# Performance work log

Measured on AMD Instinct MI355X. Metric: run time of the kernel, lower is better.

The kernel has to match this reference:

```python
import jax, jax.numpy as jnp
import numpy as np

BS, NQ, L = 64, 900, 1024
LANG_DIM, HID = 768, 256
N_EXP, TOP_K = 8, 2
MOE_W = 0.5
LOG_SCALE0 = 0.0
PRIOR_PROB = 0.01
BIAS0 = -np.log((1.0 - PRIOR_PROB) / PRIOR_PROB)  # -log((1-p)/p)


def setup_inputs() -> dict:
    key = jax.random.key(0)
    ks = jax.random.split(key, 8)
    s_in = 1.0 / np.sqrt(LANG_DIM)
    return {
        "x": jax.random.normal(ks[0], (BS, NQ, HID), jnp.float32),
        "embedding": jax.random.normal(ks[1], (BS, L, LANG_DIM), jnp.float32),
        "proj_w": jax.random.uniform(ks[2], (LANG_DIM, HID), jnp.float32, -s_in, s_in),
        "proj_b": jnp.zeros((HID,), jnp.float32),
        "gate_w": jax.random.uniform(ks[3], (LANG_DIM, N_EXP), jnp.float32, -s_in, s_in),
        "gate_b": jnp.zeros((N_EXP,), jnp.float32),
        "expert_w": jax.random.uniform(ks[4], (N_EXP, LANG_DIM, HID), jnp.float32, -s_in, s_in),
        "expert_b": jnp.zeros((N_EXP, HID), jnp.float32),
        "bias_lang": jnp.zeros((LANG_DIM,), jnp.float32),
        "bias0": jnp.array([BIAS0], jnp.float32),
        "log_scale": jnp.array([LOG_SCALE0], jnp.float32),
    }


def _moe(emb, gate_w, gate_b, expert_w, expert_b):
    # emb: (bs, L, lang_dim)
    gate_logits = emb @ gate_w + gate_b              # (bs, L, E)
    gate_weights = jax.nn.softmax(gate_logits, axis=-1)
    topv, topi = jax.lax.top_k(gate_weights, TOP_K)  # (bs, L, k)
    # dense combine weights: scatter top-k probs back to (bs, L, E)
    combine = jnp.sum(jax.nn.one_hot(topi, N_EXP, dtype=emb.dtype) * topv[..., None], axis=-2)
    out = jnp.zeros(emb.shape[:-1] + (HID,), emb.dtype)
    for e in range(N_EXP):  # small fixed expert count; dense per-expert GEMM
        out = out + combine[..., e:e + 1] * (emb @ expert_w[e] + expert_b[e])
    return out


def reference(x, embedding, proj_w, proj_b, gate_w, gate_b,
              expert_w, expert_b, bias_lang, bias0, log_scale):
    emb = embedding / jnp.linalg.norm(embedding, axis=-1, keepdims=True)
    tokens = emb @ proj_w + proj_b                        # (bs, L, HID)
    moe_out = _moe(emb, gate_w, gate_b, expert_w, expert_b)
    tokens = (1.0 - MOE_W) * tokens + MOE_W * moe_out
    token_bias = emb @ bias_lang + bias0[0]               # (bs, L)
    logit = jnp.einsum('bqh,blh->bql', x, tokens) / jnp.exp(log_scale[0])
    logit = logit + token_bias[:, None, :]
    logit = jnp.clip(logit, -50000.0, 50000.0)
    return logit
```

## Files before the change

### kernel.cpp

```cpp
#include <hip/hip_runtime.h>
#include <hip/hip_bf16.h>


typedef __attribute__((ext_vector_type(8))) short bf16x8;
typedef __attribute__((ext_vector_type(4))) float f32x4;

#define NROW 65536
#define CAP  65536
#define CSTRIDE 16

__device__ __forceinline__ unsigned short f2bf(float f) {
    unsigned u = __builtin_bit_cast(unsigned, f);
    u += 0x7fffu + ((u >> 16) & 1u);
    return (unsigned short)(u >> 16);
}
__device__ __forceinline__ float bf2f(unsigned short h) {
    unsigned u = ((unsigned)h) << 16;
    return __builtin_bit_cast(float, u);
}
__device__ __forceinline__ void gload16(const void* g, void* l) {
    __builtin_amdgcn_global_load_lds(
        (const __attribute__((address_space(1))) void*)g,
        (__attribute__((address_space(3))) void*)l, 16, 0, 0);
}
__device__ __forceinline__ unsigned cvt_pk_bf16(float a, float b) {
    unsigned r;
    asm("v_cvt_pk_bf16_f32 %0, %1, %2" : "=v"(r) : "v"(a), "v"(b));
    return r;
}

__global__ __launch_bounds__(256) void kx_cast(
    const float* __restrict__ x, unsigned short* __restrict__ x_bf)
{
    int i = blockIdx.x * 256 + threadIdx.x;
    float4 v = ((const float4*)x)[i];
    uint2 o = { cvt_pk_bf16(v.x, v.y), cvt_pk_bf16(v.z, v.w) };
    ((uint2*)x_bf)[i] = o;
}

__global__ __launch_bounds__(256) void k0_wT(
    const float* __restrict__ proj_w, const float* __restrict__ expert_w,
    unsigned short* __restrict__ wcatT)
{
    int j = blockIdx.z;
    int d0 = blockIdx.x * 64, h0 = blockIdx.y * 64;
    const float* W = (j < 8) ? expert_w + (size_t)j * 768 * 256 : proj_w;
    __shared__ unsigned short s[64][65];
    int t = threadIdx.x;
    #pragma unroll
    for (int i = 0; i < 16; i++) {
        int d = i * 4 + (t >> 6), h = t & 63;
        s[d][h] = f2bf(W[(size_t)(d0 + d) * 256 + h0 + h]);
    }
    __syncthreads();
    #pragma unroll
    for (int i = 0; i < 16; i++) {
        int h = i * 4 + (t >> 6), d = t & 63;
        wcatT[(size_t)(j * 256 + h0 + h) * 768 + d0 + d] = s[d][h];
    }
}

__global__ __launch_bounds__(256) void kz_misc(
    const float* __restrict__ proj_b, const float* __restrict__ expert_b,
    float* __restrict__ bcat, unsigned* __restrict__ cnt)
{
    int i = blockIdx.x * 256 + threadIdx.x;
    if (i < 2304) {
        int jj = i >> 8, h = i & 255;
        bcat[i] = (jj < 8) ? expert_b[jj * 256 + h] : proj_b[h];
    }
    if (i < 8 * CSTRIDE) cnt[i] = 0;
}

__global__ __launch_bounds__(256, 4) void k1_fused(
    const float* __restrict__ emb_in, const float* __restrict__ gate_w,
    const float* __restrict__ gate_b, const float* __restrict__ bias_lang,
    const float* __restrict__ bias0, unsigned short* __restrict__ emb_bf,
    unsigned* __restrict__ top2, float2* __restrict__ c2,
    float* __restrict__ tbias)
{
    __shared__ float gwT[9 * 768];
    for (int i = threadIdx.x; i < 768 * 8; i += 256) {
        int d = i >> 3, e = i & 7;
        gwT[e * 768 + d] = gate_w[i];
    }
    for (int i = threadIdx.x; i < 768; i += 256)
        gwT[8 * 768 + i] = bias_lang[i];
    __syncthreads();

    int w = threadIdx.x >> 6, lane = threadIdx.x & 63;
    #pragma unroll 1
    for (int it = 0; it < 8; ++it) {
        int r = blockIdx.x * 32 + w * 8 + it;
        const float4* rv = (const float4*)(emb_in + (size_t)r * 768);
        float4 v0 = rv[lane], v1 = rv[lane + 64], v2 = rv[lane + 128];
        float ss = v0.x*v0.x + v0.y*v0.y + v0.z*v0.z + v0.w*v0.w
                 + v1.x*v1.x + v1.y*v1.y + v1.z*v1.z + v1.w*v1.w
                 + v2.x*v2.x + v2.y*v2.y + v2.z*v2.z + v2.w*v2.w;
        #pragma unroll
        for (int m = 1; m < 64; m <<= 1) ss += __shfl_xor(ss, m, 64);
        float rn = rsqrtf(ss);

        uint2 o0 = { cvt_pk_bf16(v0.x*rn, v0.y*rn), cvt_pk_bf16(v0.z*rn, v0.w*rn) };
        uint2 o1 = { cvt_pk_bf16(v1.x*rn, v1.y*rn), cvt_pk_bf16(v1.z*rn, v1.w*rn) };
        uint2 o2 = { cvt_pk_bf16(v2.x*rn, v2.y*rn), cvt_pk_bf16(v2.z*rn, v2.w*rn) };
        uint2* ob = (uint2*)(emb_bf + (size_t)r * 768);
        ob[lane] = o0; ob[lane + 64] = o1; ob[lane + 128] = o2;

        float acc[9];
        #pragma unroll
        for (int i = 0; i < 9; i++) acc[i] = 0.f;
        const float4 vv[3] = { v0, v1, v2 };
        #pragma unroll
        for (int k = 0; k < 3; k++) {
            float4 v = vv[k];
            #pragma unroll
            for (int e = 0; e < 9; e++) {
                float4 g = *(const float4*)&gwT[e * 768 + k * 256 + lane * 4];
                acc[e] += v.x*g.x + v.y*g.y + v.z*g.z + v.w*g.w;
            }
        }
        #pragma unroll
        for (int m = 1; m < 64; m <<= 1) {
            #pragma unroll
            for (int i = 0; i < 9; i++) acc[i] += __shfl_xor(acc[i], m, 64);
        }
        if (lane == 0) {
            float g[8];
            #pragma unroll
            for (int e = 0; e < 8; e++) g[e] = acc[e] * rn + gate_b[e];
            float mx = g[0];
            #pragma unroll
            for (int e = 1; e < 8; e++) mx = fmaxf(mx, g[e]);
            float p[8], s = 0.f;
            #pragma unroll
            for (int e = 0; e < 8; e++) { p[e] = __expf(g[e] - mx); s += p[e]; }
            float inv = 0.5f / s;
            int i1 = 0;
            #pragma unroll
            for (int e = 1; e < 8; e++) if (g[e] > g[i1]) i1 = e;
            int i2 = (i1 == 0) ? 1 : 0;
            #pragma unroll
            for (int e = 0; e < 8; e++) if (e != i1 && g[e] > g[i2]) i2 = e;
            top2[r] = (unsigned)i1 | ((unsigned)i2 << 8);
            c2[r]   = make_float2(p[i1] * inv, p[i2] * inv);
            tbias[r] = acc[8] * rn + bias0[0];
        }
    }
}

__global__ __launch_bounds__(256) void kb_bucket(
    const unsigned* __restrict__ top2, const float2* __restrict__ c2,
    unsigned* __restrict__ cnt, unsigned* __restrict__ bidx,
    float* __restrict__ bscale)
{
    __shared__ unsigned lcnt[8];
    __shared__ unsigned gbase[8];
    int tid = threadIdx.x, lane = tid & 63;
    if (tid < 8) lcnt[tid] = 0;
    __syncthreads();
    int r = blockIdx.x * 256 + tid;
    unsigned t = top2[r];
    float2 c = c2[r];
    int ii[2] = { (int)(t & 255), (int)((t >> 8) & 255) };
    float cc[2] = { c.x, c.y };
    unsigned lpos[2];
    #pragma unroll
    for (int slot = 0; slot < 2; slot++) {
        int myE = ii[slot];
        #pragma unroll 1
        for (int e = 0; e < 8; e++) {
            unsigned long long mask = __ballot(myE == e);
            if (myE == e) {
                int leader = __ffsll((unsigned long long)mask) - 1;
                unsigned base = 0;
                if (lane == leader)
                    base = atomicAdd(&lcnt[e], (unsigned)__popcll(mask));
                base = __shfl(base, leader, 64);
                lpos[slot] = base + (unsigned)__popcll(mask & ((1ull << lane) - 1ull));
            }
        }
    }
    __syncthreads();
    if (tid < 8) gbase[tid] = atomicAdd(&cnt[tid * CSTRIDE], lcnt[tid]);
    __syncthreads();
    #pragma unroll
    for (int slot = 0; slot < 2; slot++) {
        int e = ii[slot];
        unsigned p = gbase[e] + lpos[slot];
        bidx[(size_t)e * CAP + p]   = (unsigned)r | ((unsigned)slot << 16);
        bscale[(size_t)e * CAP + p] = cc[slot];
    }
}

__global__ __launch_bounds__(512, 2) void k2_expert(
    const unsigned short* __restrict__ emb_bf, const unsigned short* __restrict__ wcatT,
    const float* __restrict__ bcat, const unsigned* __restrict__ cnt,
    const unsigned* __restrict__ bidx, const float* __restrict__ bscale,
    unsigned short* __restrict__ partial)
{
    int e = blockIdx.y;
    int tile = blockIdx.x;
    int cnt_e = (e < 8) ? (int)cnt[e * CSTRIDE] : NROW;
    if (tile * 128 >= cnt_e) return;
    int tid = threadIdx.x, lane = tid & 63, w = tid >> 6;
    int wm = w >> 2, wn = w & 3;
    __shared__ __align__(16) unsigned short As[2][128 * 32];
    __shared__ __align__(16) unsigned short Bs[2][256 * 32];
    __shared__ unsigned sRow[128];
    __shared__ float sScale[128];
    if (tid < 128) {
        int gi = tile * 128 + tid;
        unsigned rs; float sc;
        if (e == 8)           { rs = (unsigned)gi | (2u << 16); sc = 0.5f; }
        else if (gi < cnt_e)  { rs = bidx[(size_t)e * CAP + gi];
                                sc = bscale[(size_t)e * CAP + gi]; }
        else                  { rs = 0; sc = 0.f; }
        sRow[tid] = rs; sScale[tid] = sc;
    }
    __syncthreads();
    int r16 = lane & 15, r4 = lane >> 4;
    int srowA = tid >> 2, ssegA = (tid & 3) ^ (srowA & 3);
    const unsigned short* aSrc =
        emb_bf + (size_t)(sRow[srowA] & 0xFFFFu) * 768 + ssegA * 8;
    const unsigned short* bBase = wcatT + (size_t)e * 256 * 768;

    auto stageA = [&](int kt, int buf) {
        gload16(aSrc + kt * 32, &As[buf][w * 512]);
    };
    auto stageB = [&](int kt, int buf) {
        #pragma unroll
        for (int i = 0; i < 2; i++) {
            int u = i * 512 + tid;
            int brow = u >> 2, seg = (u & 3) ^ (brow & 3);
            gload16(&bBase[(size_t)brow * 768 + kt * 32 + seg * 8],
                    &Bs[buf][i * 4096 + w * 512]);
        }
    };

    f32x4 acc[4][4];
    #pragma unroll
    for (int mi = 0; mi < 4; mi++)
        #pragma unroll
        for (int ni = 0; ni < 4; ni++) acc[mi][ni] = f32x4{0.f, 0.f, 0.f, 0.f};

    stageA(0, 0); stageB(0, 0);
    __syncthreads();
    int buf = 0;
    #pragma unroll 1
    for (int kt = 0; kt < 24; ++kt) {
        if (kt < 23) { stageA(kt + 1, buf ^ 1); stageB(kt + 1, buf ^ 1); }
        bf16x8 a[4], b[4];
        #pragma unroll
        for (int mi = 0; mi < 4; mi++) {
            int arow = wm * 64 + mi * 16 + r16;
            a[mi] = *(const bf16x8*)&As[buf][arow * 32 + (r4 ^ (arow & 3)) * 8];
        }
        #pragma unroll
        for (int ni = 0; ni < 4; ni++) {
            int brow = wn * 64 + ni * 16 + r16;
            b[ni] = *(const bf16x8*)&Bs[buf][brow * 32 + (r4 ^ (brow & 3)) * 8];
        }
        #pragma unroll
        for (int mi = 0; mi < 4; mi++)
            #pragma unroll
            for (int ni = 0; ni < 4; ni++)
                acc[mi][ni] = __builtin_amdgcn_mfma_f32_16x16x32_bf16(
                    a[mi], b[ni], acc[mi][ni], 0, 0, 0);
        __syncthreads();
        buf ^= 1;
    }

    float bj[4];
    #pragma unroll
    for (int ni = 0; ni < 4; ni++) bj[ni] = bcat[e * 256 + wn * 64 + ni * 16 + r16];
    #pragma unroll
    for (int mi = 0; mi < 4; mi++) {
        #pragma unroll
        for (int e4 = 0; e4 < 4; e4++) {
            int rl = wm * 64 + mi * 16 + r4 * 4 + e4;
            if (tile * 128 + rl < cnt_e) {
                unsigned rs = sRow[rl];
                float sc = sScale[rl];
                unsigned rowg = rs & 0xFFFFu, slot = rs >> 16;
                #pragma unroll
                for (int ni = 0; ni < 4; ni++) {
                    int col = wn * 64 + ni * 16 + r16;
                    partial[((size_t)slot * NROW + rowg) * 256 + col] =
                        f2bf(sc * (acc[mi][ni][e4] + bj[ni]));
                }
            }
        }
    }
}

__global__ __launch_bounds__(256) void k2_combine(
    const unsigned short* __restrict__ partial, unsigned short* __restrict__ tokens)
{
    size_t i = ((size_t)blockIdx.x * 256 + threadIdx.x) * 8;
    const size_t S = (size_t)NROW * 256;
    bf16x8 p0 = *(const bf16x8*)&partial[i];
    bf16x8 p1 = *(const bf16x8*)&partial[S + i];
    bf16x8 p2 = *(const bf16x8*)&partial[2 * S + i];
    union { bf16x8 v; unsigned short s[8]; } o;
    #pragma unroll
    for (int e = 0; e < 8; e++)
        o.s[e] = f2bf(bf2f((unsigned short)p0[e]) + bf2f((unsigned short)p1[e]) +
                      bf2f((unsigned short)p2[e]));
    *(bf16x8*)&tokens[i] = o.v;
}

__global__ __launch_bounds__(256, 3) void k3_logit(
    const unsigned short* __restrict__ x_bf, const unsigned short* __restrict__ tokens,
    const float* __restrict__ tbias, const float* __restrict__ log_scale,
    float* __restrict__ out)
{
    int tid = threadIdx.x, lane = tid & 63, w = tid >> 6;
    int wm = w >> 1, wn = w & 1;
    int tn = blockIdx.x, tm = blockIdx.y, b = blockIdx.z;
    __shared__ __align__(16) unsigned short As[2][128 * 32];
    __shared__ __align__(16) unsigned short Bs[2][128 * 32];
    const unsigned short* A = x_bf + (size_t)b * 900 * 256;
    const unsigned short* B = tokens + (size_t)b * 1024 * 256;
    f32x4 acc[4][4];
    #pragma unroll
    for (int mi = 0; mi < 4; mi++)
        #pragma unroll
        for (int ni = 0; ni < 4; ni++) acc[mi][ni] = f32x4{0.f, 0.f, 0.f, 0.f};
    int r16 = lane & 15, r4 = lane >> 4;

    auto stage = [&](int kt, int buf) {
        #pragma unroll
        for (int i = 0; i < 2; i++) {
            int u = i * 256 + tid;
            int row = u >> 2, seg = (u & 3) ^ (row & 3);
            int ar = tm * 128 + row;
            if (ar > 899) ar = 899;
            gload16(&A[(size_t)ar * 256 + kt * 32 + seg * 8],
                    &As[buf][i * 2048 + w * 512]);
            int nr = tn * 128 + row;
            gload16(&B[(size_t)nr * 256 + kt * 32 + seg * 8],
                    &Bs[buf][i * 2048 + w * 512]);
        }
    };

    stage(0, 0);
    __syncthreads();
    int buf = 0;
    #pragma unroll 1
    for (int kt = 0; kt < 8; ++kt) {
        if (kt < 7) stage(kt + 1, buf ^ 1);
        bf16x8 a[4], bb[4];
        #pragma unroll
        for (int mi = 0; mi < 4; mi++) {
            int row = wm * 64 + mi * 16 + r16;
            a[mi] = *(const bf16x8*)&As[buf][row * 32 + (r4 ^ (row & 3)) * 8];
        }
        #pragma unroll
        for (int ni = 0; ni < 4; ni++) {
            int row = wn * 64 + ni * 16 + r16;
            bb[ni] = *(const bf16x8*)&Bs[buf][row * 32 + (r4 ^ (row & 3)) * 8];
        }
        #pragma unroll
        for (int mi = 0; mi < 4; mi++)
            #pragma unroll
            for (int ni = 0; ni < 4; ni++)
                acc[mi][ni] = __builtin_amdgcn_mfma_f32_16x16x32_bf16(
                    a[mi], bb[ni], acc[mi][ni], 0, 0, 0);
        __syncthreads();
        buf ^= 1;
    }
    float inv = __expf(-log_scale[0]);
    #pragma unroll
    for (int ni = 0; ni < 4; ni++) {
        int l = tn * 128 + wn * 64 + ni * 16 + r16;
        float tbv = tbias[b * 1024 + l];
        #pragma unroll
        for (int mi = 0; mi < 4; mi++) {
            #pragma unroll
            for (int e = 0; e < 4; e++) {
                int q = tm * 128 + wm * 64 + mi * 16 + r4 * 4 + e;
                if (q < 900) {
                    float vv = acc[mi][ni][e] * inv + tbv;
                    vv = fminf(fmaxf(vv, -50000.f), 50000.f);
                    out[((size_t)b * 900 + q) * 1024 + l] = vv;
                }
            }
        }
    }
}

extern "C" void kernel_launch(void* const* d_in, const int* in_sizes, int n_in,
                              void* d_out, int out_size, void* d_ws, size_t ws_size,
                              hipStream_t stream)
{
    const float* x         = (const float*)d_in[0];
    const float* embedding = (const float*)d_in[1];
    const float* proj_w    = (const float*)d_in[2];
    const float* proj_b    = (const float*)d_in[3];
    const float* gate_w    = (const float*)d_in[4];
    const float* gate_b    = (const float*)d_in[5];
    const float* expert_w  = (const float*)d_in[6];
    const float* expert_b  = (const float*)d_in[7];
    const float* bias_lang = (const float*)d_in[8];
    const float* bias0     = (const float*)d_in[9];
    const float* log_scale = (const float*)d_in[10];
    float* out = (float*)d_out;

    size_t off = 0;
    char* base = (char*)d_ws;
    auto alloc = [&](size_t bytes) -> void* {
        void* p = base + off;
        off += (bytes + 255) & ~(size_t)255;
        return p;
    };
    unsigned short* emb_bf  = (unsigned short*)alloc((size_t)NROW * 768 * 2);
    unsigned short* x_bf    = (unsigned short*)alloc((size_t)14745600 * 2);
    unsigned short* wcatT   = (unsigned short*)alloc((size_t)2304 * 768 * 2);
    float* bcat             = (float*)alloc(2304 * 4);
    float* tbias            = (float*)alloc((size_t)NROW * 4);
    unsigned short* tokens  = (unsigned short*)alloc((size_t)NROW * 256 * 2);
    unsigned* cnt           = (unsigned*)alloc(8 * CSTRIDE * 4);
    unsigned* top2          = (unsigned*)alloc((size_t)NROW * 4);
    float2* c2              = (float2*)alloc((size_t)NROW * 8);
    unsigned* bidx          = (unsigned*)alloc((size_t)8 * CAP * 4);
    float* bscale           = (float*)alloc((size_t)8 * CAP * 4);
    unsigned short* partial = (unsigned short*)alloc((size_t)3 * NROW * 256 * 2);

    kx_cast<<<14400, 256, 0, stream>>>(x, x_bf);
    dim3 gt(12, 4, 9);
    k0_wT<<<gt, 256, 0, stream>>>(proj_w, expert_w, wcatT);
    kz_misc<<<9, 256, 0, stream>>>(proj_b, expert_b, bcat, cnt);
    k1_fused<<<2048, 256, 0, stream>>>(embedding, gate_w, gate_b, bias_lang, bias0,
                                       emb_bf, top2, c2, tbias);
    kb_bucket<<<NROW / 256, 256, 0, stream>>>(top2, c2, cnt, bidx, bscale);
    dim3 g2(512, 9);
    k2_expert<<<g2, 512, 0, stream>>>(emb_bf, wcatT, bcat, cnt, bidx, bscale, partial);
    k2_combine<<<8192, 256, 0, stream>>>(partial, tokens);
    dim3 g3(8, 8, 64);
    k3_logit<<<g3, 256, 0, stream>>>(x_bf, tokens, tbias, log_scale, out);
}
```

Measured before the change: 395.9 us.

## Triple-buffer LDS staging with partial vmcnt waits in expert and logit GEMMs

Both GEMM kernels move from double- to triple-buffered LDS tiles, prefetching two K-steps ahead. The full __syncthreads is replaced by a partial s_waitcnt vmcnt plus s_barrier, so the next tile's global-to-LDS loads can stay in flight across the barrier. This is meant to hide global load latency behind MFMA work. In exchange, LDS use per block grows by half, which may reduce occupancy (k2 goes to about 72KB per block), and the hand-coded vmcnt counts must match the number of issued loads exactly.

Result: slower. 415.3 us (+4.9%).

```diff
diff --git a/kernel.cpp b/kernel.cpp
--- a/kernel.cpp
+++ b/kernel.cpp
@@ -205,8 +205,8 @@
     if (tile * 128 >= cnt_e) return;
     int tid = threadIdx.x, lane = tid & 63, w = tid >> 6;
     int wm = w >> 2, wn = w & 3;
-    __shared__ __align__(16) unsigned short As[2][128 * 32];
-    __shared__ __align__(16) unsigned short Bs[2][256 * 32];
+    __shared__ __align__(16) unsigned short As[3][128 * 32];
+    __shared__ __align__(16) unsigned short Bs[3][256 * 32];
     __shared__ unsigned sRow[128];
     __shared__ float sScale[128];
     if (tid < 128) {
@@ -245,21 +245,25 @@
         for (int ni = 0; ni < 4; ni++) acc[mi][ni] = f32x4{0.f, 0.f, 0.f, 0.f};
 
     stageA(0, 0); stageB(0, 0);
-    __syncthreads();
-    int buf = 0;
+    stageA(1, 1); stageB(1, 1);
+    asm volatile("s_waitcnt vmcnt(3)" ::: "memory");
+    __builtin_amdgcn_s_barrier();
+
+    int rb = 0;
     #pragma unroll 1
     for (int kt = 0; kt < 24; ++kt) {
-        if (kt < 23) { stageA(kt + 1, buf ^ 1); stageB(kt + 1, buf ^ 1); }
+        int sb = rb + 2; if (sb >= 3) sb -= 3;
+        if (kt < 22) { stageA(kt + 2, sb); stageB(kt + 2, sb); }
         bf16x8 a[4], b[4];
         #pragma unroll
         for (int mi = 0; mi < 4; mi++) {
             int arow = wm * 64 + mi * 16 + r16;
-            a[mi] = *(const bf16x8*)&As[buf][arow * 32 + (r4 ^ (arow & 3)) * 8];
+            a[mi] = *(const bf16x8*)&As[rb][arow * 32 + (r4 ^ (arow & 3)) * 8];
         }
         #pragma unroll
         for (int ni = 0; ni < 4; ni++) {
             int brow = wn * 64 + ni * 16 + r16;
-            b[ni] = *(const bf16x8*)&Bs[buf][brow * 32 + (r4 ^ (brow & 3)) * 8];
+            b[ni] = *(const bf16x8*)&Bs[rb][brow * 32 + (r4 ^ (brow & 3)) * 8];
         }
         #pragma unroll
         for (int mi = 0; mi < 4; mi++)
@@ -267,8 +271,12 @@
             for (int ni = 0; ni < 4; ni++)
                 acc[mi][ni] = __builtin_amdgcn_mfma_f32_16x16x32_bf16(
                     a[mi], b[ni], acc[mi][ni], 0, 0, 0);
-        __syncthreads();
-        buf ^= 1;
+        if (kt < 23) {
+            if (kt == 22) asm volatile("s_waitcnt vmcnt(0)" ::: "memory");
+            else          asm volatile("s_waitcnt vmcnt(3)" ::: "memory");
+            __builtin_amdgcn_s_barrier();
+        }
+        rb = rb + 1; if (rb >= 3) rb = 0;
     }
 
     float bj[4];
@@ -318,8 +326,8 @@
     int tid = threadIdx.x, lane = tid & 63, w = tid >> 6;
     int wm = w >> 1, wn = w & 1;
     int tn = blockIdx.x, tm = blockIdx.y, b = blockIdx.z;
-    __shared__ __align__(16) unsigned short As[2][128 * 32];
-    __shared__ __align__(16) unsigned short Bs[2][128 * 32];
+    __shared__ __align__(16) unsigned short As[3][128 * 32];
+    __shared__ __align__(16) unsigned short Bs[3][128 * 32];
     const unsigned short* A = x_bf + (size_t)b * 900 * 256;
     const unsigned short* B = tokens + (size_t)b * 1024 * 256;
     f32x4 acc[4][4];
@@ -345,21 +353,25 @@
     };
 
     stage(0, 0);
-    __syncthreads();
-    int buf = 0;
+    stage(1, 1);
+    asm volatile("s_waitcnt vmcnt(4)" ::: "memory");
+    __builtin_amdgcn_s_barrier();
+
+    int rb = 0;
     #pragma unroll 1
     for (int kt = 0; kt < 8; ++kt) {
-        if (kt < 7) stage(kt + 1, buf ^ 1);
+        int sb = rb + 2; if (sb >= 3) sb -= 3;
+        if (kt < 6) stage(kt + 2, sb);
         bf16x8 a[4], bb[4];
         #pragma unroll
         for (int mi = 0; mi < 4; mi++) {
             int row = wm * 64 + mi * 16 + r16;
-            a[mi] = *(const bf16x8*)&As[buf][row * 32 + (r4 ^ (row & 3)) * 8];
+            a[mi] = *(const bf16x8*)&As[rb][row * 32 + (r4 ^ (row & 3)) * 8];
         }
         #pragma unroll
         for (int ni = 0; ni < 4; ni++) {
             int row = wn * 64 + ni * 16 + r16;
-            bb[ni] = *(const bf16x8*)&Bs[buf][row * 32 + (r4 ^ (row & 3)) * 8];
+            bb[ni] = *(const bf16x8*)&Bs[rb][row * 32 + (r4 ^ (row & 3)) * 8];
         }
         #pragma unroll
         for (int mi = 0; mi < 4; mi++)
@@ -367,8 +379,12 @@
             for (int ni = 0; ni < 4; ni++)
                 acc[mi][ni] = __builtin_amdgcn_mfma_f32_16x16x32_bf16(
                     a[mi], bb[ni], acc[mi][ni], 0, 0, 0);
-        __syncthreads();
-        buf ^= 1;
+        if (kt < 7) {
+            if (kt == 6) asm volatile("s_waitcnt vmcnt(0)" ::: "memory");
+            else         asm volatile("s_waitcnt vmcnt(4)" ::: "memory");
+            __builtin_amdgcn_s_barrier();
+        }
+        rb = rb + 1; if (rb >= 3) rb = 0;
     }
     float inv = __expf(-log_scale[0]);
     #pragma unroll
```

## Fuse projection GEMM with partial combine, add nontemporal stores and stronger LDS swizzle

Applied to the files above, without the earlier changes.

Removes the separate combine kernel by moving the projection GEMM (former expert slot 8) into a dedicated kernel that adds the two expert partials in its epilogue. This drops one partial buffer and a full read/write pass over the tokens. The change also widens the LDS XOR swizzle to mix in more row bits, makes the large output and intermediate writes nontemporal, and raises k3_logit occupancy to 4 blocks. The risks are a serialized projection kernel in place of one overlapped inside the expert grid, plus possible register pressure at the higher occupancy.

Result: no change. 393.8 us (-0.5%).

```diff
diff --git a/kernel.cpp b/kernel.cpp
--- a/kernel.cpp
+++ b/kernel.cpp
@@ -8,6 +8,7 @@
 #define NROW 65536
 #define CAP  65536
 #define CSTRIDE 16
+#define SWZ(r) ((((r) & 3) ^ (((r) >> 2) & 3)))
 
 __device__ __forceinline__ unsigned short f2bf(float f) {
     unsigned u = __builtin_bit_cast(unsigned, f);
@@ -34,8 +35,9 @@
 {
     int i = blockIdx.x * 256 + threadIdx.x;
     float4 v = ((const float4*)x)[i];
-    uint2 o = { cvt_pk_bf16(v.x, v.y), cvt_pk_bf16(v.z, v.w) };
-    ((uint2*)x_bf)[i] = o;
+    unsigned long long o = (unsigned long long)cvt_pk_bf16(v.x, v.y) |
+                           ((unsigned long long)cvt_pk_bf16(v.z, v.w) << 32);
+    __builtin_nontemporal_store(o, (unsigned long long*)x_bf + i);
 }
 
 __global__ __launch_bounds__(256) void k0_wT(
@@ -101,11 +103,16 @@
         for (int m = 1; m < 64; m <<= 1) ss += __shfl_xor(ss, m, 64);
         float rn = rsqrtf(ss);
 
-        uint2 o0 = { cvt_pk_bf16(v0.x*rn, v0.y*rn), cvt_pk_bf16(v0.z*rn, v0.w*rn) };
-        uint2 o1 = { cvt_pk_bf16(v1.x*rn, v1.y*rn), cvt_pk_bf16(v1.z*rn, v1.w*rn) };
-        uint2 o2 = { cvt_pk_bf16(v2.x*rn, v2.y*rn), cvt_pk_bf16(v2.z*rn, v2.w*rn) };
-        uint2* ob = (uint2*)(emb_bf + (size_t)r * 768);
-        ob[lane] = o0; ob[lane + 64] = o1; ob[lane + 128] = o2;
+        unsigned long long q0 = (unsigned long long)cvt_pk_bf16(v0.x*rn, v0.y*rn) |
+                                ((unsigned long long)cvt_pk_bf16(v0.z*rn, v0.w*rn) << 32);
+        unsigned long long q1 = (unsigned long long)cvt_pk_bf16(v1.x*rn, v1.y*rn) |
+                                ((unsigned long long)cvt_pk_bf16(v1.z*rn, v1.w*rn) << 32);
+        unsigned long long q2 = (unsigned long long)cvt_pk_bf16(v2.x*rn, v2.y*rn) |
+                                ((unsigned long long)cvt_pk_bf16(v2.z*rn, v2.w*rn) << 32);
+        unsigned long long* ob = (unsigned long long*)(emb_bf + (size_t)r * 768);
+        __builtin_nontemporal_store(q0, ob + lane);
+        __builtin_nontemporal_store(q1, ob + lane + 64);
+        __builtin_nontemporal_store(q2, ob + lane + 128);
 
         float acc[9];
         #pragma unroll
@@ -201,7 +208,7 @@
 {
     int e = blockIdx.y;
     int tile = blockIdx.x;
-    int cnt_e = (e < 8) ? (int)cnt[e * CSTRIDE] : NROW;
+    int cnt_e = (int)cnt[e * CSTRIDE];
     if (tile * 128 >= cnt_e) return;
     int tid = threadIdx.x, lane = tid & 63, w = tid >> 6;
     int wm = w >> 2, wn = w & 3;
@@ -212,15 +219,14 @@
     if (tid < 128) {
         int gi = tile * 128 + tid;
         unsigned rs; float sc;
-        if (e == 8)           { rs = (unsigned)gi | (2u << 16); sc = 0.5f; }
-        else if (gi < cnt_e)  { rs = bidx[(size_t)e * CAP + gi];
-                                sc = bscale[(size_t)e * CAP + gi]; }
-        else                  { rs = 0; sc = 0.f; }
+        if (gi < cnt_e) { rs = bidx[(size_t)e * CAP + gi];
+                          sc = bscale[(size_t)e * CAP + gi]; }
+        else            { rs = 0; sc = 0.f; }
         sRow[tid] = rs; sScale[tid] = sc;
     }
     __syncthreads();
     int r16 = lane & 15, r4 = lane >> 4;
-    int srowA = tid >> 2, ssegA = (tid & 3) ^ (srowA & 3);
+    int srowA = tid >> 2, ssegA = (tid & 3) ^ SWZ(srowA);
     const unsigned short* aSrc =
         emb_bf + (size_t)(sRow[srowA] & 0xFFFFu) * 768 + ssegA * 8;
     const unsigned short* bBase = wcatT + (size_t)e * 256 * 768;
@@ -232,7 +238,7 @@
         #pragma unroll
         for (int i = 0; i < 2; i++) {
             int u = i * 512 + tid;
-            int brow = u >> 2, seg = (u & 3) ^ (brow & 3);
+            int brow = u >> 2, seg = (u & 3) ^ SWZ(brow);
             gload16(&bBase[(size_t)brow * 768 + kt * 32 + seg * 8],
                     &Bs[buf][i * 4096 + w * 512]);
         }
@@ -254,12 +260,12 @@
         #pragma unroll
         for (int mi = 0; mi < 4; mi++) {
             int arow = wm * 64 + mi * 16 + r16;
-            a[mi] = *(const bf16x8*)&As[buf][arow * 32 + (r4 ^ (arow & 3)) * 8];
+            a[mi] = *(const bf16x8*)&As[buf][arow * 32 + (r4 ^ SWZ(arow)) * 8];
         }
         #pragma unroll
         for (int ni = 0; ni < 4; ni++) {
             int brow = wn * 64 + ni * 16 + r16;
-            b[ni] = *(const bf16x8*)&Bs[buf][brow * 32 + (r4 ^ (brow & 3)) * 8];
+            b[ni] = *(const bf16x8*)&Bs[buf][brow * 32 + (r4 ^ SWZ(brow)) * 8];
         }
         #pragma unroll
         for (int mi = 0; mi < 4; mi++)
@@ -286,31 +292,101 @@
                 #pragma unroll
                 for (int ni = 0; ni < 4; ni++) {
                     int col = wn * 64 + ni * 16 + r16;
-                    partial[((size_t)slot * NROW + rowg) * 256 + col] =
-                        f2bf(sc * (acc[mi][ni][e4] + bj[ni]));
+                    __builtin_nontemporal_store(
+                        f2bf(sc * (acc[mi][ni][e4] + bj[ni])),
+                        &partial[((size_t)slot * NROW + rowg) * 256 + col]);
                 }
             }
         }
     }
 }
 
-__global__ __launch_bounds__(256) void k2_combine(
-    const unsigned short* __restrict__ partial, unsigned short* __restrict__ tokens)
-{
-    size_t i = ((size_t)blockIdx.x * 256 + threadIdx.x) * 8;
+__global__ __launch_bounds__(512, 2) void k2_proj(
+    const unsigned short* __restrict__ emb_bf, const unsigned short* __restrict__ wcatT,
+    const float* __restrict__ bcat, const unsigned short* __restrict__ partial,
+    unsigned short* __restrict__ tokens)
+{
+    int tile = blockIdx.x;
+    int tid = threadIdx.x, lane = tid & 63, w = tid >> 6;
+    int wm = w >> 2, wn = w & 3;
+    int rowBase = tile * 128;
+    __shared__ __align__(16) unsigned short As[2][128 * 32];
+    __shared__ __align__(16) unsigned short Bs[2][256 * 32];
+    int r16 = lane & 15, r4 = lane >> 4;
+    int srowA = tid >> 2, ssegA = (tid & 3) ^ SWZ(srowA);
+    const unsigned short* aSrc =
+        emb_bf + (size_t)(rowBase + srowA) * 768 + ssegA * 8;
+    const unsigned short* bBase = wcatT + (size_t)8 * 256 * 768;
+
+    auto stageA = [&](int kt, int buf) {
+        gload16(aSrc + kt * 32, &As[buf][w * 512]);
+    };
+    auto stageB = [&](int kt, int buf) {
+        #pragma unroll
+        for (int i = 0; i < 2; i++) {
+            int u = i * 512 + tid;
+            int brow = u >> 2, seg = (u & 3) ^ SWZ(brow);
+            gload16(&bBase[(size_t)brow * 768 + kt * 32 + seg * 8],
+                    &Bs[buf][i * 4096 + w * 512]);
+        }
+    };
+
+    f32x4 acc[4][4];
+    #pragma unroll
+    for (int mi = 0; mi < 4; mi++)
+        #pragma unroll
+        for (int ni = 0; ni < 4; ni++) acc[mi][ni] = f32x4{0.f, 0.f, 0.f, 0.f};
+
+    stageA(0, 0); stageB(0, 0);
+    __syncthreads();
+    int buf = 0;
+    #pragma unroll 1
+    for (int kt = 0; kt < 24; ++kt) {
+        if (kt < 23) { stageA(kt + 1, buf ^ 1); stageB(kt + 1, buf ^ 1); }
+        bf16x8 a[4], b[4];
+        #pragma unroll
+        for (int mi = 0; mi < 4; mi++) {
+            int arow = wm * 64 + mi * 16 + r16;
+            a[mi] = *(const bf16x8*)&As[buf][arow * 32 + (r4 ^ SWZ(arow)) * 8];
+        }
+        #pragma unroll
+        for (int ni = 0; ni < 4; ni++) {
+            int brow = wn * 64 + ni * 16 + r16;
+            b[ni] = *(const bf16x8*)&Bs[buf][brow * 32 + (r4 ^ SWZ(brow)) * 8];
+        }
+        #pragma unroll
+        for (int mi = 0; mi < 4; mi++)
+            #pragma unroll
+            for (int ni = 0; ni < 4; ni++)
+                acc[mi][ni] = __builtin_amdgcn_mfma_f32_16x16x32_bf16(
+                    a[mi], b[ni], acc[mi][ni], 0, 0, 0);
+        __syncthreads();
+        buf ^= 1;
+    }
+
     const size_t S = (size_t)NROW * 256;
-    bf16x8 p0 = *(const bf16x8*)&partial[i];
-    bf16x8 p1 = *(const bf16x8*)&partial[S + i];
-    bf16x8 p2 = *(const bf16x8*)&partial[2 * S + i];
-    union { bf16x8 v; unsigned short s[8]; } o;
-    #pragma unroll
-    for (int e = 0; e < 8; e++)
-        o.s[e] = f2bf(bf2f((unsigned short)p0[e]) + bf2f((unsigned short)p1[e]) +
-                      bf2f((unsigned short)p2[e]));
-    *(bf16x8*)&tokens[i] = o.v;
-}
-
-__global__ __launch_bounds__(256, 3) void k3_logit(
+    float bj[4];
+    #pragma unroll
+    for (int ni = 0; ni < 4; ni++) bj[ni] = bcat[8 * 256 + wn * 64 + ni * 16 + r16];
+    #pragma unroll
+    for (int mi = 0; mi < 4; mi++) {
+        #pragma unroll
+        for (int e4 = 0; e4 < 4; e4++) {
+            int rl = wm * 64 + mi * 16 + r4 * 4 + e4;
+            size_t rowg = rowBase + rl;
+            #pragma unroll
+            for (int ni = 0; ni < 4; ni++) {
+                int col = wn * 64 + ni * 16 + r16;
+                float p0 = bf2f(partial[rowg * 256 + col]);
+                float p1 = bf2f(partial[S + rowg * 256 + col]);
+                float v = 0.5f * (acc[mi][ni][e4] + bj[ni]) + p0 + p1;
+                __builtin_nontemporal_store(f2bf(v), &tokens[rowg * 256 + col]);
+            }
+        }
+    }
+}
+
+__global__ __launch_bounds__(256, 4) void k3_logit(
     const unsigned short* __restrict__ x_bf, const unsigned short* __restrict__ tokens,
     const float* __restrict__ tbias, const float* __restrict__ log_scale,
     float* __restrict__ out)
@@ -333,7 +409,7 @@
         #pragma unroll
         for (int i = 0; i < 2; i++) {
             int u = i * 256 + tid;
-            int row = u >> 2, seg = (u & 3) ^ (row & 3);
+            int row = u >> 2, seg = (u & 3) ^ SWZ(row);
             int ar = tm * 128 + row;
             if (ar > 899) ar = 899;
             gload16(&A[(size_t)ar * 256 + kt * 32 + seg * 8],
@@ -354,12 +430,12 @@
         #pragma unroll
         for (int mi = 0; mi < 4; mi++) {
             int row = wm * 64 + mi * 16 + r16;
-            a[mi] = *(const bf16x8*)&As[buf][row * 32 + (r4 ^ (row & 3)) * 8];
+            a[mi] = *(const bf16x8*)&As[buf][row * 32 + (r4 ^ SWZ(row)) * 8];
         }
         #pragma unroll
         for (int ni = 0; ni < 4; ni++) {
             int row = wn * 64 + ni * 16 + r16;
-            bb[ni] = *(const bf16x8*)&Bs[buf][row * 32 + (r4 ^ (row & 3)) * 8];
+            bb[ni] = *(const bf16x8*)&Bs[buf][row * 32 + (r4 ^ SWZ(row)) * 8];
         }
         #pragma unroll
         for (int mi = 0; mi < 4; mi++)
@@ -383,7 +459,8 @@
                 if (q < 900) {
                     float vv = acc[mi][ni][e] * inv + tbv;
                     vv = fminf(fmaxf(vv, -50000.f), 50000.f);
-                    out[((size_t)b * 900 + q) * 1024 + l] = vv;
+                    __builtin_nontemporal_store(
+                        vv, &out[((size_t)b * 900 + q) * 1024 + l]);
                 }
             }
         }
@@ -425,7 +502,7 @@
     float2* c2              = (float2*)alloc((size_t)NROW * 8);
     unsigned* bidx          = (unsigned*)alloc((size_t)8 * CAP * 4);
     float* bscale           = (float*)alloc((size_t)8 * CAP * 4);
-    unsigned short* partial = (unsigned short*)alloc((size_t)3 * NROW * 256 * 2);
+    unsigned short* partial = (unsigned short*)alloc((size_t)2 * NROW * 256 * 2);
 
     kx_cast<<<14400, 256, 0, stream>>>(x, x_bf);
     dim3 gt(12, 4, 9);
@@ -434,9 +511,9 @@
     k1_fused<<<2048, 256, 0, stream>>>(embedding, gate_w, gate_b, bias_lang, bias0,
                                        emb_bf, top2, c2, tbias);
     kb_bucket<<<NROW / 256, 256, 0, stream>>>(top2, c2, cnt, bidx, bscale);
-    dim3 g2(512, 9);
+    dim3 g2(512, 8);
     k2_expert<<<g2, 512, 0, stream>>>(emb_bf, wcatT, bcat, cnt, bidx, bscale, partial);
-    k2_combine<<<8192, 256, 0, stream>>>(partial, tokens);
+    k2_proj<<<512, 512, 0, stream>>>(emb_bf, wcatT, bcat, partial, tokens);
     dim3 g3(8, 8, 64);
     k3_logit<<<g3, 256, 0, stream>>>(x_bf, tokens, tbias, log_scale, out);
 }
```

## Bucket rows by expert pair and fuse three-GEMM combine in registers

Applied to the files above, without the earlier changes.

Rows are bucketed by their ordered top-2 expert pair (64 keys) instead of per expert. Each row tile now runs the two expert GEMMs plus the projection GEMM back to back and combines them in registers. This removes the 3-slot partial buffer and the separate combine kernel, along with their global traffic. The change also adds nontemporal stores, an XCD-aware block remap and a wider LDS swizzle in the logit kernel, and raises its occupancy hint. A fixed per-pair capacity (CAP2) silently drops rows when a pair exceeds it, and partially filled tiles across many buckets waste some MFMA work.

Measured after the change: 472.7 us. 19.4% more time.

```diff
diff --git a/kernel.cpp b/kernel.cpp
--- a/kernel.cpp
+++ b/kernel.cpp
@@ -6,8 +6,9 @@
 typedef __attribute__((ext_vector_type(4))) float f32x4;
 
 #define NROW 65536
-#define CAP  65536
+#define CAP2 6144
 #define CSTRIDE 16
+#define SWZ(r) ((((r) & 3) ^ (((r) >> 2) & 3)))
 
 __device__ __forceinline__ unsigned short f2bf(float f) {
     unsigned u = __builtin_bit_cast(unsigned, f);
@@ -34,8 +35,9 @@
 {
     int i = blockIdx.x * 256 + threadIdx.x;
     float4 v = ((const float4*)x)[i];
-    uint2 o = { cvt_pk_bf16(v.x, v.y), cvt_pk_bf16(v.z, v.w) };
-    ((uint2*)x_bf)[i] = o;
+    unsigned long long o = (unsigned long long)cvt_pk_bf16(v.x, v.y) |
+                           ((unsigned long long)cvt_pk_bf16(v.z, v.w) << 32);
+    __builtin_nontemporal_store(o, (unsigned long long*)x_bf + i);
 }
 
 __global__ __launch_bounds__(256) void k0_wT(
@@ -69,7 +71,7 @@
         int jj = i >> 8, h = i & 255;
         bcat[i] = (jj < 8) ? expert_b[jj * 256 + h] : proj_b[h];
     }
-    if (i < 8 * CSTRIDE) cnt[i] = 0;
+    if (i < 64 * CSTRIDE) cnt[i] = 0;
 }
 
 __global__ __launch_bounds__(256, 4) void k1_fused(
@@ -101,11 +103,16 @@
         for (int m = 1; m < 64; m <<= 1) ss += __shfl_xor(ss, m, 64);
         float rn = rsqrtf(ss);
 
-        uint2 o0 = { cvt_pk_bf16(v0.x*rn, v0.y*rn), cvt_pk_bf16(v0.z*rn, v0.w*rn) };
-        uint2 o1 = { cvt_pk_bf16(v1.x*rn, v1.y*rn), cvt_pk_bf16(v1.z*rn, v1.w*rn) };
-        uint2 o2 = { cvt_pk_bf16(v2.x*rn, v2.y*rn), cvt_pk_bf16(v2.z*rn, v2.w*rn) };
-        uint2* ob = (uint2*)(emb_bf + (size_t)r * 768);
-        ob[lane] = o0; ob[lane + 64] = o1; ob[lane + 128] = o2;
+        unsigned long long q0 = (unsigned long long)cvt_pk_bf16(v0.x*rn, v0.y*rn) |
+                                ((unsigned long long)cvt_pk_bf16(v0.z*rn, v0.w*rn) << 32);
+        unsigned long long q1 = (unsigned long long)cvt_pk_bf16(v1.x*rn, v1.y*rn) |
+                                ((unsigned long long)cvt_pk_bf16(v1.z*rn, v1.w*rn) << 32);
+        unsigned long long q2 = (unsigned long long)cvt_pk_bf16(v2.x*rn, v2.y*rn) |
+                                ((unsigned long long)cvt_pk_bf16(v2.z*rn, v2.w*rn) << 32);
+        unsigned long long* ob = (unsigned long long*)(emb_bf + (size_t)r * 768);
+        __builtin_nontemporal_store(q0, ob + lane);
+        __builtin_nontemporal_store(q1, ob + lane + 64);
+        __builtin_nontemporal_store(q2, ob + lane + 128);
 
         float acc[9];
         #pragma unroll
@@ -152,172 +159,160 @@
 __global__ __launch_bounds__(256) void kb_bucket(
     const unsigned* __restrict__ top2, const float2* __restrict__ c2,
     unsigned* __restrict__ cnt, unsigned* __restrict__ bidx,
-    float* __restrict__ bscale)
-{
-    __shared__ unsigned lcnt[8];
-    __shared__ unsigned gbase[8];
-    int tid = threadIdx.x, lane = tid & 63;
-    if (tid < 8) lcnt[tid] = 0;
+    float2* __restrict__ bscale2)
+{
+    __shared__ unsigned lcnt[64];
+    __shared__ unsigned gbase[64];
+    int tid = threadIdx.x;
+    if (tid < 64) lcnt[tid] = 0;
     __syncthreads();
     int r = blockIdx.x * 256 + tid;
     unsigned t = top2[r];
-    float2 c = c2[r];
-    int ii[2] = { (int)(t & 255), (int)((t >> 8) & 255) };
-    float cc[2] = { c.x, c.y };
-    unsigned lpos[2];
-    #pragma unroll
-    for (int slot = 0; slot < 2; slot++) {
-        int myE = ii[slot];
-        #pragma unroll 1
-        for (int e = 0; e < 8; e++) {
-            unsigned long long mask = __ballot(myE == e);
-            if (myE == e) {
-                int leader = __ffsll((unsigned long long)mask) - 1;
-                unsigned base = 0;
-                if (lane == leader)
-                    base = atomicAdd(&lcnt[e], (unsigned)__popcll(mask));
-                base = __shfl(base, leader, 64);
-                lpos[slot] = base + (unsigned)__popcll(mask & ((1ull << lane) - 1ull));
-            }
-        }
-    }
-    __syncthreads();
-    if (tid < 8) gbase[tid] = atomicAdd(&cnt[tid * CSTRIDE], lcnt[tid]);
-    __syncthreads();
-    #pragma unroll
-    for (int slot = 0; slot < 2; slot++) {
-        int e = ii[slot];
-        unsigned p = gbase[e] + lpos[slot];
-        bidx[(size_t)e * CAP + p]   = (unsigned)r | ((unsigned)slot << 16);
-        bscale[(size_t)e * CAP + p] = cc[slot];
-    }
-}
-
-__global__ __launch_bounds__(512, 2) void k2_expert(
+    int key = (int)((t & 255) * 8 + ((t >> 8) & 255));
+    unsigned lpos = atomicAdd(&lcnt[key], 1u);
+    __syncthreads();
+    if (tid < 64)
+        gbase[tid] = lcnt[tid] ? atomicAdd(&cnt[tid * CSTRIDE], lcnt[tid]) : 0u;
+    __syncthreads();
+    unsigned p = gbase[key] + lpos;
+    if (p < CAP2) {
+        bidx[(size_t)key * CAP2 + p]    = (unsigned)r;
+        bscale2[(size_t)key * CAP2 + p] = c2[r];
+    }
+}
+
+__global__ __launch_bounds__(512, 2) void k2_pair(
     const unsigned short* __restrict__ emb_bf, const unsigned short* __restrict__ wcatT,
     const float* __restrict__ bcat, const unsigned* __restrict__ cnt,
-    const unsigned* __restrict__ bidx, const float* __restrict__ bscale,
-    unsigned short* __restrict__ partial)
-{
-    int e = blockIdx.y;
-    int tile = blockIdx.x;
-    int cnt_e = (e < 8) ? (int)cnt[e * CSTRIDE] : NROW;
-    if (tile * 128 >= cnt_e) return;
+    const unsigned* __restrict__ bidx, const float2* __restrict__ bscale2,
+    unsigned short* __restrict__ tokens)
+{
+    int key = blockIdx.y, tile = blockIdx.x;
+    int cnt_k = (int)cnt[key * CSTRIDE];
+    if (cnt_k > CAP2) cnt_k = CAP2;
+    if (tile * 128 >= cnt_k) return;
     int tid = threadIdx.x, lane = tid & 63, w = tid >> 6;
     int wm = w >> 2, wn = w & 3;
-    __shared__ __align__(16) unsigned short As[2][128 * 32];
+    __shared__ __align__(16) unsigned short As[12 * 4096];
     __shared__ __align__(16) unsigned short Bs[2][256 * 32];
     __shared__ unsigned sRow[128];
-    __shared__ float sScale[128];
+    __shared__ float2 sC[128];
     if (tid < 128) {
         int gi = tile * 128 + tid;
-        unsigned rs; float sc;
-        if (e == 8)           { rs = (unsigned)gi | (2u << 16); sc = 0.5f; }
-        else if (gi < cnt_e)  { rs = bidx[(size_t)e * CAP + gi];
-                                sc = bscale[(size_t)e * CAP + gi]; }
-        else                  { rs = 0; sc = 0.f; }
-        sRow[tid] = rs; sScale[tid] = sc;
+        if (gi < cnt_k) { sRow[tid] = bidx[(size_t)key * CAP2 + gi];
+                          sC[tid]   = bscale2[(size_t)key * CAP2 + gi]; }
+        else            { sRow[tid] = 0; sC[tid] = make_float2(0.f, 0.f); }
     }
     __syncthreads();
     int r16 = lane & 15, r4 = lane >> 4;
-    int srowA = tid >> 2, ssegA = (tid & 3) ^ (srowA & 3);
-    const unsigned short* aSrc =
-        emb_bf + (size_t)(sRow[srowA] & 0xFFFFu) * 768 + ssegA * 8;
-    const unsigned short* bBase = wcatT + (size_t)e * 256 * 768;
-
-    auto stageA = [&](int kt, int buf) {
-        gload16(aSrc + kt * 32, &As[buf][w * 512]);
-    };
-    auto stageB = [&](int kt, int buf) {
+    int arow = tid >> 2, aseg = (tid & 3) ^ SWZ(arow);
+    const unsigned short* aSrc = emb_bf + (size_t)sRow[arow] * 768 + aseg * 8;
+    int jmap[3] = { key >> 3, key & 7, 8 };
+
+    auto stageB = [&](int e, int half, int kt, int bbuf) {
         #pragma unroll
         for (int i = 0; i < 2; i++) {
             int u = i * 512 + tid;
-            int brow = u >> 2, seg = (u & 3) ^ (brow & 3);
-            gload16(&bBase[(size_t)brow * 768 + kt * 32 + seg * 8],
-                    &Bs[buf][i * 4096 + w * 512]);
+            int brow = u >> 2, seg = (u & 3) ^ SWZ(brow);
+            gload16(&wcatT[((size_t)e * 256 + brow) * 768 + half * 384 + kt * 32 + seg * 8],
+                    &Bs[bbuf][i * 4096 + w * 512]);
         }
     };
 
-    f32x4 acc[4][4];
+    f32x4 fin[4][4];
     #pragma unroll
     for (int mi = 0; mi < 4; mi++)
         #pragma unroll
-        for (int ni = 0; ni < 4; ni++) acc[mi][ni] = f32x4{0.f, 0.f, 0.f, 0.f};
-
-    stageA(0, 0); stageB(0, 0);
-    __syncthreads();
-    int buf = 0;
+        for (int ni = 0; ni < 4; ni++) fin[mi][ni] = f32x4{0.f, 0.f, 0.f, 0.f};
+
     #pragma unroll 1
-    for (int kt = 0; kt < 24; ++kt) {
-        if (kt < 23) { stageA(kt + 1, buf ^ 1); stageB(kt + 1, buf ^ 1); }
-        bf16x8 a[4], b[4];
-        #pragma unroll
-        for (int mi = 0; mi < 4; mi++) {
-            int arow = wm * 64 + mi * 16 + r16;
-            a[mi] = *(const bf16x8*)&As[buf][arow * 32 + (r4 ^ (arow & 3)) * 8];
-        }
-        #pragma unroll
-        for (int ni = 0; ni < 4; ni++) {
-            int brow = wn * 64 + ni * 16 + r16;
-            b[ni] = *(const bf16x8*)&Bs[buf][brow * 32 + (r4 ^ (brow & 3)) * 8];
-        }
-        #pragma unroll
-        for (int mi = 0; mi < 4; mi++)
+    for (int half = 0; half < 2; ++half) {
+        #pragma unroll
+        for (int kt = 0; kt < 12; kt++)
+            gload16(aSrc + half * 384 + kt * 32, &As[kt * 4096 + w * 512]);
+        stageB(jmap[0], half, 0, 0);
+        __syncthreads();
+        int buf = 0;
+        #pragma unroll 1
+        for (int j = 0; j < 3; ++j) {
+            f32x4 acc[4][4];
+            #pragma unroll
+            for (int mi = 0; mi < 4; mi++)
+                #pragma unroll
+                for (int ni = 0; ni < 4; ni++) acc[mi][ni] = f32x4{0.f, 0.f, 0.f, 0.f};
+            #pragma unroll 1
+            for (int kt = 0; kt < 12; ++kt) {
+                int p = j * 12 + kt;
+                if (p < 35) { int np = p + 1; stageB(jmap[np / 12], half, np % 12, buf ^ 1); }
+                bf16x8 a[4], b[4];
+                #pragma unroll
+                for (int mi = 0; mi < 4; mi++) {
+                    int ar = wm * 64 + mi * 16 + r16;
+                    a[mi] = *(const bf16x8*)&As[kt * 4096 + ar * 32 + (r4 ^ SWZ(ar)) * 8];
+                }
+                #pragma unroll
+                for (int ni = 0; ni < 4; ni++) {
+                    int br = wn * 64 + ni * 16 + r16;
+                    b[ni] = *(const bf16x8*)&Bs[buf][br * 32 + (r4 ^ SWZ(br)) * 8];
+                }
+                #pragma unroll
+                for (int mi = 0; mi < 4; mi++)
+                    #pragma unroll
+                    for (int ni = 0; ni < 4; ni++)
+                        acc[mi][ni] = __builtin_amdgcn_mfma_f32_16x16x32_bf16(
+                            a[mi], b[ni], acc[mi][ni], 0, 0, 0);
+                __syncthreads();
+                buf ^= 1;
+            }
+            float bj[4];
             #pragma unroll
             for (int ni = 0; ni < 4; ni++)
-                acc[mi][ni] = __builtin_amdgcn_mfma_f32_16x16x32_bf16(
-                    a[mi], b[ni], acc[mi][ni], 0, 0, 0);
-        __syncthreads();
-        buf ^= 1;
-    }
-
-    float bj[4];
-    #pragma unroll
-    for (int ni = 0; ni < 4; ni++) bj[ni] = bcat[e * 256 + wn * 64 + ni * 16 + r16];
+                bj[ni] = half ? bcat[jmap[j] * 256 + wn * 64 + ni * 16 + r16] : 0.f;
+            #pragma unroll
+            for (int mi = 0; mi < 4; mi++) {
+                #pragma unroll
+                for (int e4 = 0; e4 < 4; e4++) {
+                    int rl = wm * 64 + mi * 16 + r4 * 4 + e4;
+                    float c = (j == 0) ? sC[rl].x : (j == 1) ? sC[rl].y : 0.5f;
+                    #pragma unroll
+                    for (int ni = 0; ni < 4; ni++)
+                        fin[mi][ni][e4] += c * (acc[mi][ni][e4] + bj[ni]);
+                }
+            }
+        }
+    }
+
     #pragma unroll
     for (int mi = 0; mi < 4; mi++) {
         #pragma unroll
         for (int e4 = 0; e4 < 4; e4++) {
             int rl = wm * 64 + mi * 16 + r4 * 4 + e4;
-            if (tile * 128 + rl < cnt_e) {
-                unsigned rs = sRow[rl];
-                float sc = sScale[rl];
-                unsigned rowg = rs & 0xFFFFu, slot = rs >> 16;
+            if (tile * 128 + rl < cnt_k) {
+                size_t rowg = sRow[rl];
                 #pragma unroll
                 for (int ni = 0; ni < 4; ni++) {
                     int col = wn * 64 + ni * 16 + r16;
-                    partial[((size_t)slot * NROW + rowg) * 256 + col] =
-                        f2bf(sc * (acc[mi][ni][e4] + bj[ni]));
+                    __builtin_nontemporal_store(f2bf(fin[mi][ni][e4]),
+                                                &tokens[rowg * 256 + col]);
                 }
             }
         }
     }
 }
 
-__global__ __launch_bounds__(256) void k2_combine(
-    const unsigned short* __restrict__ partial, unsigned short* __restrict__ tokens)
-{
-    size_t i = ((size_t)blockIdx.x * 256 + threadIdx.x) * 8;
-    const size_t S = (size_t)NROW * 256;
-    bf16x8 p0 = *(const bf16x8*)&partial[i];
-    bf16x8 p1 = *(const bf16x8*)&partial[S + i];
-    bf16x8 p2 = *(const bf16x8*)&partial[2 * S + i];
-    union { bf16x8 v; unsigned short s[8]; } o;
-    #pragma unroll
-    for (int e = 0; e < 8; e++)
-        o.s[e] = f2bf(bf2f((unsigned short)p0[e]) + bf2f((unsigned short)p1[e]) +
-                      bf2f((unsigned short)p2[e]));
-    *(bf16x8*)&tokens[i] = o.v;
-}
-
-__global__ __launch_bounds__(256, 3) void k3_logit(
+__global__ __launch_bounds__(256, 4) void k3_logit(
     const unsigned short* __restrict__ x_bf, const unsigned short* __restrict__ tokens,
     const float* __restrict__ tbias, const float* __restrict__ log_scale,
     float* __restrict__ out)
 {
+    int wgid = blockIdx.x;
+    int xcd = wgid & 7, slot = wgid >> 3;
+    int b = xcd + 8 * (slot >> 6);
+    int t64 = slot & 63;
+    int tm = t64 >> 3, tn = t64 & 7;
+
     int tid = threadIdx.x, lane = tid & 63, w = tid >> 6;
     int wm = w >> 1, wn = w & 1;
-    int tn = blockIdx.x, tm = blockIdx.y, b = blockIdx.z;
     __shared__ __align__(16) unsigned short As[2][128 * 32];
     __shared__ __align__(16) unsigned short Bs[2][128 * 32];
     const unsigned short* A = x_bf + (size_t)b * 900 * 256;
@@ -333,7 +328,7 @@
         #pragma unroll
         for (int i = 0; i < 2; i++) {
             int u = i * 256 + tid;
-            int row = u >> 2, seg = (u & 3) ^ (row & 3);
+            int row = u >> 2, seg = (u & 3) ^ SWZ(row);
             int ar = tm * 128 + row;
             if (ar > 899) ar = 899;
             gload16(&A[(size_t)ar * 256 + kt * 32 + seg * 8],
@@ -354,12 +349,12 @@
         #pragma unroll
         for (int mi = 0; mi < 4; mi++) {
             int row = wm * 64 + mi * 16 + r16;
-            a[mi] = *(const bf16x8*)&As[buf][row * 32 + (r4 ^ (row & 3)) * 8];
+            a[mi] = *(const bf16x8*)&As[buf][row * 32 + (r4 ^ SWZ(row)) * 8];
         }
         #pragma unroll
         for (int ni = 0; ni < 4; ni++) {
             int row = wn * 64 + ni * 16 + r16;
-            bb[ni] = *(const bf16x8*)&Bs[buf][row * 32 + (r4 ^ (row & 3)) * 8];
+            bb[ni] = *(const bf16x8*)&Bs[buf][row * 32 + (r4 ^ SWZ(row)) * 8];
         }
         #pragma unroll
         for (int mi = 0; mi < 4; mi++)
@@ -383,7 +378,8 @@
                 if (q < 900) {
                     float vv = acc[mi][ni][e] * inv + tbv;
                     vv = fminf(fmaxf(vv, -50000.f), 50000.f);
-                    out[((size_t)b * 900 + q) * 1024 + l] = vv;
+                    __builtin_nontemporal_store(
+                        vv, &out[((size_t)b * 900 + q) * 1024 + l]);
                 }
             }
         }
@@ -420,12 +416,11 @@
     float* bcat             = (float*)alloc(2304 * 4);
     float* tbias            = (float*)alloc((size_t)NROW * 4);
     unsigned short* tokens  = (unsigned short*)alloc((size_t)NROW * 256 * 2);
-    unsigned* cnt           = (unsigned*)alloc(8 * CSTRIDE * 4);
+    unsigned* cnt           = (unsigned*)alloc(64 * CSTRIDE * 4);
     unsigned* top2          = (unsigned*)alloc((size_t)NROW * 4);
     float2* c2              = (float2*)alloc((size_t)NROW * 8);
-    unsigned* bidx          = (unsigned*)alloc((size_t)8 * CAP * 4);
-    float* bscale           = (float*)alloc((size_t)8 * CAP * 4);
-    unsigned short* partial = (unsigned short*)alloc((size_t)3 * NROW * 256 * 2);
+    unsigned* bidx          = (unsigned*)alloc((size_t)64 * CAP2 * 4);
+    float2* bscale2         = (float2*)alloc((size_t)64 * CAP2 * 8);
 
     kx_cast<<<14400, 256, 0, stream>>>(x, x_bf);
     dim3 gt(12, 4, 9);
@@ -433,10 +428,8 @@
     kz_misc<<<9, 256, 0, stream>>>(proj_b, expert_b, bcat, cnt);
     k1_fused<<<2048, 256, 0, stream>>>(embedding, gate_w, gate_b, bias_lang, bias0,
                                        emb_bf, top2, c2, tbias);
-    kb_bucket<<<NROW / 256, 256, 0, stream>>>(top2, c2, cnt, bidx, bscale);
-    dim3 g2(512, 9);
-    k2_expert<<<g2, 512, 0, stream>>>(emb_bf, wcatT, bcat, cnt, bidx, bscale, partial);
-    k2_combine<<<8192, 256, 0, stream>>>(partial, tokens);
-    dim3 g3(8, 8, 64);
-    k3_logit<<<g3, 256, 0, stream>>>(x_bf, tokens, tbias, log_scale, out);
-}
+    kb_bucket<<<NROW / 256, 256, 0, stream>>>(top2, c2, cnt, bidx, bscale2);
+    dim3 g2(CAP2 / 128, 64);
+    k2_pair<<<g2, 512, 0, stream>>>(emb_bf, wcatT, bcat, cnt, bidx, bscale2, tokens);
+    k3_logit<<<4096, 256, 0, stream>>>(x_bf, tokens, tbias, log_scale, out);
+}
```
